# Performance work log

Measured on AMD Instinct MI355X. Metric: run time of the kernel, lower is better.

## Reference

```python
import jax, jax.numpy as jnp
import numpy as np

B, T, C, K = 8, 4096, 256, 4  # batch, time, d_embd, k_periods


def setup_inputs() -> dict:
    key = jax.random.key(0)
    ks = jax.random.split(key, 5)
    x = jax.random.normal(ks[0], (B, T, C), jnp.float32)
    # inception stand-in: masked 3x3 conv (HWIO) + GELU
    Wc = jax.random.normal(ks[1], (3, 3, C, C), jnp.float32) * 0.02
    bc = jnp.zeros((C,), jnp.float32)
    # FeedForward params
    W1 = jax.random.normal(ks[2], (C, 4 * C), jnp.float32) * 0.02
    b1 = jnp.zeros((4 * C,), jnp.float32)
    W2 = jax.random.normal(ks[3], (4 * C, C), jnp.float32) * 0.02
    b2 = jnp.zeros((C,), jnp.float32)
    return {"x": x, "Wc": Wc, "bc": bc, "W1": W1, "b1": b1, "W2": W2, "b2": b2}


def _topk_freq_idx(x):
    # eager (concrete) period detection; shapes downstream are data-dependent,
    # exactly like the torch original (which is also not compilable as one graph)
    xf = jnp.fft.rfft(x, axis=1)[:, 1:, :]            # drop DC -> [B, T//2, C]
    amps_full = jnp.mean(jnp.abs(xf), axis=-1)        # [B, T//2]
    _, idx = jax.lax.top_k(amps_full, K)              # [B, K] indices into sliced bins
    return np.asarray(jax.device_get(idx))


def _fold(x, n):
    # vectorized per-sample 1D->2D folding with period n[b]; returns masked grid
    pad = (T - T % n) % n
    m = (T + pad) // n
    M, N = int(m.max()), int(n.max())
    nj = jnp.asarray(n)[:, None, None]                # [B,1,1]
    i = jnp.arange(M)[None, :, None]
    j = jnp.arange(N)[None, None, :]
    t = i * nj + j                                    # [B,M,N] flat time index
    valid = (j < nj) & (t < T)
    tc = jnp.clip(t, 0, T - 1)
    grid = x[jnp.arange(B)[:, None, None], tc] * valid[..., None]  # [B,M,N,C]
    mask = valid[..., None].astype(x.dtype)
    return grid, mask


def _inception(grid, mask, Wc, bc):
    y = jax.lax.conv_general_dilated(
        grid, Wc, window_strides=(1, 1), padding='SAME',
        dimension_numbers=('NHWC', 'HWIO', 'NHWC'))
    return jax.nn.gelu(y + bc, approximate=False) * mask


def _unfold(y, n):
    ts = jnp.arange(T)[None, :]
    nj = jnp.asarray(n)[:, None]
    return y[jnp.arange(B)[:, None], ts // nj, ts % nj]  # [B,T,C]


def _forward(x, Wc, bc, W1, b1, W2, b2, idx_np):
    # differentiable amplitude recomputation with fixed (closed-over) indices
    xf = jnp.fft.rfft(x, axis=1)[:, 1:, :]
    amps_full = jnp.mean(jnp.abs(xf), axis=-1)                     # [B, T//2]
    amps_k = jnp.take_along_axis(amps_full, jnp.asarray(idx_np), axis=1)  # [B,K]
    # original computes p = T // topk_index; clamp to avoid div-by-zero on idx 0
    p = np.maximum(T // np.maximum(idx_np, 1), 1)                   # [B,K] np ints
    outs = []
    for k in range(K):
        grid, mask = _fold(x, p[:, k])
        y = _inception(grid, mask, Wc, bc)
        outs.append(_unfold(y, p[:, k]))
    tf = jnp.stack(outs, axis=1)                                   # [B,K,T,C]
    h = jax.nn.gelu(tf @ W1 + b1, approximate=False) @ W2 + b2     # FeedForward
    w = jax.nn.softmax(amps_k, axis=-1)[:, :, None, None]
    return x + (h * w).sum(axis=1)


def reference(x, Wc, bc, W1, b1, W2, b2):
    idx_np = _topk_freq_idx(x)
    return _forward(x, Wc, bc, W1, b1, W2, b2, idx_np)
```

## Files before the change

### kernel.cpp

```cpp
#include <hip/hip_runtime.h>
#include <cstdint>
#include <cstddef>

#define T_LEN 4096
#define C_DIM 256
#define B_DIM 8
#define K_TOP 4

typedef __attribute__((ext_vector_type(8))) short bf16x8;
typedef __attribute__((ext_vector_type(4))) float f32x4;

__device__ __forceinline__ float gelu_fast(float x) {
    float x2 = x * x;
    float a = x * fmaf(0.071354816f, x2, 1.595769122f);
    float e = __expf(-a);
    return __fdividef(x, 1.0f + e);
}

__device__ __forceinline__ unsigned short f2bf(float f) {
    uint32_t u = __float_as_uint(f);
    uint32_t r = (u + 0x7fffu + ((u >> 16) & 1u)) >> 16;
    return (unsigned short)r;
}

__device__ __forceinline__ float bf2f(unsigned short v) {
    uint32_t u = ((uint32_t)v) << 16;
    return __uint_as_float(u);
}

typedef __attribute__((address_space(3))) uint32_t lds_u32_t;
typedef __attribute__((address_space(1))) const uint32_t gbl_u32_t;

__device__ __forceinline__ void lds_load16(const void* g, void* l) {
    __builtin_amdgcn_global_load_lds((gbl_u32_t*)g, (lds_u32_t*)l, 16, 0, 0);
}

#define BAR_VM0()                                                      \
    do {                                                               \
        asm volatile("s_waitcnt vmcnt(0) lgkmcnt(0)" ::: "memory");    \
        __builtin_amdgcn_s_barrier();                                  \
        __builtin_amdgcn_sched_barrier(0);                             \
    } while (0)
#define BAR_VM3()                                                      \
    do {                                                               \
        asm volatile("s_waitcnt vmcnt(3) lgkmcnt(0)" ::: "memory");    \
        __builtin_amdgcn_s_barrier();                                  \
        __builtin_amdgcn_sched_barrier(0);                             \
    } while (0)
#define BAR_LGKM()                                                     \
    do {                                                               \
        asm volatile("s_waitcnt lgkmcnt(0)" ::: "memory");             \
        __builtin_amdgcn_s_barrier();                                  \
        __builtin_amdgcn_sched_barrier(0);                             \
    } while (0)

#define FPAD(i) ((i) + ((i) >> 5))

__global__ __launch_bounds__(256) void cvt_x_kernel(const float4* __restrict__ x,
                                                    ushort4* __restrict__ xbf,
                                                    unsigned short* __restrict__ zbuf) {
    size_t i = (size_t)blockIdx.x * 256 + threadIdx.x;
    float4 v = x[i];
    ushort4 o;
    o.x = f2bf(v.x); o.y = f2bf(v.y); o.z = f2bf(v.z); o.w = f2bf(v.w);
    xbf[i] = o;
    if (blockIdx.x == 0 && threadIdx.x < 256) zbuf[threadIdx.x] = 0;
}

__global__ __launch_bounds__(256) void transpose_cvtx_kernel(const float* __restrict__ x,
                                                             float* __restrict__ xT,
                                                             unsigned short* __restrict__ xbf,
                                                             unsigned short* __restrict__ zbuf) {
    __shared__ float tile[32][33];
    const int b = blockIdx.z;
    const int t0 = blockIdx.x * 32, c0 = blockIdx.y * 32;
    const int lx = threadIdx.x & 31, ly = threadIdx.x >> 5;
    const float* xp = x + (size_t)b * T_LEN * C_DIM;
    unsigned short* xbp = xbf + (size_t)b * T_LEN * C_DIM;
    float* op = xT + (size_t)b * C_DIM * T_LEN;
    for (int rr = ly; rr < 32; rr += 8) {
        float v = xp[(size_t)(t0 + rr) * C_DIM + c0 + lx];
        tile[rr][lx] = v;
        xbp[(size_t)(t0 + rr) * C_DIM + c0 + lx] = f2bf(v);
    }
    __syncthreads();
    for (int rr = ly; rr < 32; rr += 8)
        op[(size_t)(c0 + rr) * T_LEN + t0 + lx] = tile[lx][rr];
    if (blockIdx.x == 0 && blockIdx.y == 0 && blockIdx.z == 0)
        zbuf[threadIdx.x] = 0;
}

__global__ __launch_bounds__(256) void transpose_cvt_kernel(const float* __restrict__ src,
                                                            unsigned short* __restrict__ dst,
                                                            int R, int C) {
    __shared__ float t[32][33];
    const int c0 = blockIdx.x * 32, r0 = blockIdx.y * 32;
    const int lx = threadIdx.x & 31, ly = threadIdx.x >> 5;
    for (int rr = ly; rr < 32; rr += 8) {
        int r = r0 + rr, c = c0 + lx;
        t[rr][lx] = (r < R && c < C) ? src[(size_t)r * C + c] : 0.0f;
    }
    __syncthreads();
    for (int rr = ly; rr < 32; rr += 8) {
        int c = c0 + rr, r = r0 + lx;
        if (r < R && c < C) dst[(size_t)c * R + r] = f2bf(t[lx][rr]);
    }
}

__global__ __launch_bounds__(256) void repack_frag_kernel(const float* __restrict__ src,
                                                          unsigned short* __restrict__ dst,
                                                          int K, int N) {
    int idx = blockIdx.x * 256 + threadIdx.x;
    int total = (N >> 4) * (K >> 5) * 64;
    if (idx >= total) return;
    int lane = idx & 63, tile = idx >> 6;
    int ktiles = K >> 5;
    int tile_n = tile / ktiles, tile_k = tile % ktiles;
    int col = tile_n * 16 + (lane & 15);
    int k0 = tile_k * 32 + (lane >> 4) * 8;
    __align__(16) unsigned short v[8];
#pragma unroll
    for (int j = 0; j < 8; j++) v[j] = f2bf(src[(size_t)(k0 + j) * N + col]);
    *(uint4*)(dst + (size_t)idx * 8) = *(const uint4*)v;
}

__global__ __launch_bounds__(256) void fft_mag_kernel(const float* __restrict__ src,
                                                      unsigned short* __restrict__ mags,
                                                      int transposed) {
    const int bx = blockIdx.x;
    const int b = bx >> 8;
    const int c = bx & 255;
    const int tid = threadIdx.x;

    __shared__ __align__(16) float re[4224];
    __shared__ __align__(16) float im[4224];
    __shared__ __align__(16) float twr[2048];
    __shared__ __align__(16) float twi[2048];

    for (int u = tid; u < 2048; u += 256) {
        float ang = -6.283185307179586f * (float)u / 4096.0f;
        float s, co;
        sincosf(ang, &s, &co);
        twr[u] = co;
        twi[u] = s;
    }
    for (int i = tid; i < 4224; i += 256) im[i] = 0.0f;

    if (transposed) {
        const float4* row = (const float4*)(src + ((size_t)(b * C_DIM + c)) * T_LEN);
        for (int e4 = tid; e4 < 1024; e4 += 256) {
            float4 v = row[e4];
            int e = e4 * 4;
            re[FPAD((int)(__brev((unsigned)(e + 0)) >> 20))] = v.x;
            re[FPAD((int)(__brev((unsigned)(e + 1)) >> 20))] = v.y;
            re[FPAD((int)(__brev((unsigned)(e + 2)) >> 20))] = v.z;
            re[FPAD((int)(__brev((unsigned)(e + 3)) >> 20))] = v.w;
        }
    } else {
        const float* xp = src + (size_t)b * T_LEN * C_DIM + c;
        for (int e = tid; e < 4096; e += 256) {
            int r = (int)(__brev((unsigned)e) >> 20);
            re[FPAD(r)] = xp[(size_t)e * C_DIM];
        }
    }
    __syncthreads();

#pragma unroll
    for (int sp = 0; sp < 6; sp++) {
        const int h = 1 << (2 * sp);
        const int t1s = 11 - 2 * sp;
        const int t2s = 10 - 2 * sp;
        for (int j = tid; j < 1024; j += 256) {
            int p = j & (h - 1);
            int G = j >> (2 * sp);
            int base = G * 4 * h + p;
            int iA = FPAD(base), iB = FPAD(base + h);
            int iC = FPAD(base + 2 * h), iD = FPAD(base + 3 * h);
            float w1r = twr[p << t1s], w1i = twi[p << t1s];
            float w2r = twr[p << t2s], w2i = twi[p << t2s];
            float Ar = re[iA], Ai = im[iA], Br = re[iB], Bi = im[iB];
            float Cr = re[iC], Ci = im[iC], Dr = re[iD], Di = im[iD];
            float tBr = w1r * Br - w1i * Bi, tBi = w1r * Bi + w1i * Br;
            float tDr = w1r * Dr - w1i * Di, tDi = w1r * Di + w1i * Dr;
            float A1r = Ar + tBr, A1i = Ai + tBi;
            float B1r = Ar - tBr, B1i = Ai - tBi;
            float C1r = Cr + tDr, C1i = Ci + tDi;
            float D1r = Cr - tDr, D1i = Ci - tDi;
            float tCr = w2r * C1r - w2i * C1i, tCi = w2r * C1i + w2i * C1r;
            float uDr = w2r * D1r - w2i * D1i, uDi = w2r * D1i + w2i * D1r;
            float vDr = uDi, vDi = -uDr;
            re[iA] = A1r + tCr; im[iA] = A1i + tCi;
            re[iC] = A1r - tCr; im[iC] = A1i - tCi;
            re[iB] = B1r + vDr; im[iB] = B1i + vDi;
            re[iD] = B1r - vDr; im[iD] = B1i - vDi;
        }
        __syncthreads();
    }

    unsigned short* mp = mags + ((size_t)(b * C_DIM + c)) * 2048;
    for (int u = tid; u < 2048; u += 256) {
        int f = FPAD(u + 1);
        mp[u] = f2bf(sqrtf(re[f] * re[f] + im[f] * im[f]));
    }
}

__global__ __launch_bounds__(256) void reduce_amps_kernel(const unsigned short* __restrict__ mags,
                                                          float* __restrict__ partial) {
    const int b = blockIdx.z, cc = blockIdx.y;
    const int u = blockIdx.x * 256 + threadIdx.x;
    const unsigned short* mp = mags + ((size_t)b * C_DIM + cc * 32) * 2048 + u;
    float s = 0.0f;
    for (int c = 0; c < 32; c++) s += bf2f(mp[(size_t)c * 2048]);
    partial[((size_t)b * 8 + cc) * 2048 + u] = s;
}

__global__ __launch_bounds__(256) void topk_kernel(const float* __restrict__ partial,
                                                   int* __restrict__ meta_p,
                                                   float* __restrict__ meta_w) {
    const int b = blockIdx.x;
    const int tid = threadIdx.x;
    __shared__ float v[2048];
    __shared__ float rv[256];
    __shared__ int ri[256];
    __shared__ float topv[K_TOP];
    __shared__ int topi[K_TOP];

    for (int u = tid; u < 2048; u += 256) {
        float s = 0.0f;
        for (int cc = 0; cc < 8; cc++) s += partial[((size_t)b * 8 + cc) * 2048 + u];
        v[u] = s * (1.0f / (float)C_DIM);
    }

    for (int k = 0; k < K_TOP; k++) {
        __syncthreads();
        float bv = -1e30f;
        int bi = 2048;
        for (int u = tid; u < 2048; u += 256) {
            float val = v[u];
            if (val > bv) { bv = val; bi = u; }
        }
        rv[tid] = bv;
        ri[tid] = bi;
        __syncthreads();
        for (int s = 128; s > 0; s >>= 1) {
            if (tid < s) {
                float ov = rv[tid + s];
                int oi = ri[tid + s];
                if (ov > rv[tid] || (ov == rv[tid] && oi < ri[tid])) {
                    rv[tid] = ov;
                    ri[tid] = oi;
                }
            }
            __syncthreads();
        }
        if (tid == 0) {
            topv[k] = rv[0];
            topi[k] = ri[0];
            v[ri[0]] = -1e30f;
        }
    }
    __syncthreads();
    if (tid == 0) {
        float mx = topv[0];
        for (int k = 1; k < K_TOP; k++) mx = fmaxf(mx, topv[k]);
        float e[K_TOP], se = 0.0f;
        for (int k = 0; k < K_TOP; k++) { e[k] = expf(topv[k] - mx); se += e[k]; }
        for (int k = 0; k < K_TOP; k++) {
            int idx = topi[k];
            int d = (idx >= 1) ? idx : 1;
            int p = T_LEN / d;
            if (p < 1) p = 1;
            meta_p[b * K_TOP + k] = p;
            meta_w[b * K_TOP + k] = e[k] / se;
        }
    }
}

__global__ __launch_bounds__(512) void conv_mfma_kernel(const unsigned short* __restrict__ xbf,
                                                        const unsigned short* __restrict__ WcT,
                                                        const float* __restrict__ bc,
                                                        const int* __restrict__ meta_p,
                                                        const unsigned short* __restrict__ zbuf,
                                                        unsigned short* __restrict__ convbufs,
                                                        size_t conv_stride, int koff) {
    const int b = blockIdx.y;
    const int kz = blockIdx.z;
    const int n = meta_p[b * K_TOP + koff + kz];
    const int row0 = blockIdx.x * 128;
    const int tid = threadIdx.x, w = tid >> 6, lane = tid & 63;
    const int wm = w >> 2, wn = w & 3;

    __shared__ __align__(16) unsigned short Al[3][128 * 32];
    __shared__ __align__(16) unsigned short Bl[3][256 * 32];

    const int ra = tid >> 2;
    const int swz = ((tid & 3) ^ ((ra >> 1) & 3)) * 8;
    int ti, tj;
    {
        int t = row0 + ra;
        ti = t / n;
        tj = t - ti * n;
    }
    const unsigned short* xb = xbf + (size_t)b * T_LEN * C_DIM;
    const unsigned short* baseB0 = WcT + (size_t)ra * 2304 + swz;
    const unsigned short* baseB1 = WcT + (size_t)(ra + 128) * 2304 + swz;

    auto computeA = [&](int q) -> const unsigned short* {
        int di = q / 3 - 1, dj = q % 3 - 1;
        int ii = ti + di, jj = tj + dj;
        int tp = ii * n + jj;
        bool ok = (jj >= 0) && (jj < n) && (ii >= 0) && (tp < T_LEN);
        return ok ? (xb + (size_t)tp * C_DIM + swz) : (zbuf + swz);
    };

    f32x4 acc[4][4];
#pragma unroll
    for (int m = 0; m < 4; m++)
#pragma unroll
        for (int nn = 0; nn < 4; nn++) acc[m][nn] = (f32x4){0.f, 0.f, 0.f, 0.f};

    const unsigned short* baseA = computeA(0);
    lds_load16(baseA, &Al[0][tid * 8]);
    lds_load16(baseB0, &Bl[0][tid * 8]);
    lds_load16(baseB1, &Bl[0][4096 + tid * 8]);
    lds_load16(baseA + 32, &Al[1][tid * 8]);
    lds_load16(baseB0 + 32, &Bl[1][tid * 8]);
    lds_load16(baseB1 + 32, &Bl[1][4096 + tid * 8]);

    int cur = 0, stb = 2;
    for (int s = 0; s < 72; s++) {
        if (s < 71) BAR_VM3();
        else        BAR_VM0();

        const int t = s + 2;
        if (t < 72) {
            if ((t & 7) == 0) baseA = computeA(t >> 3);
            lds_load16(baseA + (t & 7) * 32, &Al[stb][tid * 8]);
            lds_load16(baseB0 + (size_t)t * 32, &Bl[stb][tid * 8]);
            lds_load16(baseB1 + (size_t)t * 32, &Bl[stb][4096 + tid * 8]);
        }

        bf16x8 af[4], bfr[4];
#pragma unroll
        for (int m = 0; m < 4; m++) {
            int row = wm * 64 + m * 16 + (lane & 15);
            af[m] = *(const bf16x8*)((const char*)&Al[cur][0] + row * 64 +
                                     (((lane >> 4) * 16) ^ (((row >> 1) & 3) << 4)));
        }
#pragma unroll
        for (int nn = 0; nn < 4; nn++) {
            int rowb = wn * 64 + nn * 16 + (lane & 15);
            bfr[nn] = *(const bf16x8*)((const char*)&Bl[cur][0] + rowb * 64 +
                                       (((lane >> 4) * 16) ^ (((rowb >> 1) & 3) << 4)));
        }
        __builtin_amdgcn_s_setprio(1);
#pragma unroll
        for (int m = 0; m < 4; m++)
#pragma unroll
            for (int nn = 0; nn < 4; nn++)
                acc[m][nn] = __builtin_amdgcn_mfma_f32_16x16x32_bf16(af[m], bfr[nn], acc[m][nn], 0, 0, 0);
        __builtin_amdgcn_s_setprio(0);

        cur = (cur == 2) ? 0 : cur + 1;
        stb = (stb == 2) ? 0 : stb + 1;
    }

    unsigned short* ob = convbufs + (size_t)kz * conv_stride + (size_t)b * T_LEN * C_DIM;
#pragma unroll
    for (int nn = 0; nn < 4; nn++) {
        int col = wn * 64 + nn * 16 + (lane & 15);
        float bs = bc[col];
#pragma unroll
        for (int m = 0; m < 4; m++) {
            int rbase = row0 + wm * 64 + m * 16 + (lane >> 4) * 4;
#pragma unroll
            for (int r = 0; r < 4; r++) {
                float v = acc[m][nn][r] + bs;
                ob[(size_t)(rbase + r) * C_DIM + col] = f2bf(gelu_fast(v));
            }
        }
    }
}

template <int KCNT>
__global__ __launch_bounds__(256, 2) void fused_ff_kernel(
    const unsigned short* __restrict__ convbufs, size_t conv_stride,
    const unsigned short* __restrict__ W1frag,
    const unsigned short* __restrict__ W2frag,
    const float* __restrict__ b1,
    const float* __restrict__ b2,
    const float* __restrict__ meta_w,
    float* __restrict__ out,
    const float* __restrict__ osrc,
    float b2scale, int koff) {
    const int tid = threadIdx.x;
    const int wn = tid >> 6, lane = tid & 63;
    const int row0 = blockIdx.x * 32;
    const int b = row0 >> 12;

    __shared__ __align__(16) unsigned short Asw[KCNT * 32 * 256];
    __shared__ __align__(16) unsigned short Hsw[2][32 * 128];

    float wkv[KCNT];
#pragma unroll
    for (int kc = 0; kc < KCNT; kc++) wkv[kc] = meta_w[b * K_TOP + koff + kc];

    {
        const unsigned short* base = convbufs + (size_t)row0 * C_DIM;
#pragma unroll
        for (int u = 0; u < KCNT * 4; u++) {
            int ch = u * 256 + tid;
            int rfull = ch >> 5;
            int kc = rfull >> 5;
            int trow = rfull & 31;
            int cole = ((ch & 31) * 8) ^ ((rfull & 7) << 3);
            lds_load16(base + (size_t)kc * conv_stride + (size_t)trow * 256 + cole,
                       (unsigned short*)Asw + (size_t)ch * 8);
        }
    }

    f32x4 acc2[2][4];
#pragma unroll
    for (int t2 = 0; t2 < 2; t2++)
#pragma unroll
        for (int nn = 0; nn < 4; nn++) acc2[t2][nn] = (f32x4){0.f, 0.f, 0.f, 0.f};

    BAR_VM0();

    for (int cc = 0; cc < 8; cc++) {
        const int par = cc & 1;

        f32x4 acc1[KCNT][2][2];
#pragma unroll
        for (int kc = 0; kc < KCNT; kc++)
#pragma unroll
            for (int n2 = 0; n2 < 2; n2++)
#pragma unroll
                for (int t2 = 0; t2 < 2; t2++) acc1[kc][n2][t2] = (f32x4){0.f, 0.f, 0.f, 0.f};

        __builtin_amdgcn_s_setprio(1);
#pragma unroll
        for (int ks = 0; ks < 8; ks++) {
            bf16x8 w1f[2];
#pragma unroll
            for (int n2 = 0; n2 < 2; n2++) {
                int tile_n = cc * 8 + wn * 2 + n2;
                w1f[n2] = *(const bf16x8*)(W1frag + ((size_t)(tile_n * 8 + ks) * 64 + lane) * 8);
            }
            bf16x8 af[KCNT][2];
#pragma unroll
            for (int kc = 0; kc < KCNT; kc++)
#pragma unroll
                for (int t2 = 0; t2 < 2; t2++) {
                    int row = kc * 32 + t2 * 16 + (lane & 15);
                    af[kc][t2] = *(const bf16x8*)((const char*)Asw + row * 512 +
                                                  ((ks * 64 + (lane >> 4) * 16) ^ ((row & 7) << 4)));
                }
#pragma unroll
            for (int kc = 0; kc < KCNT; kc++)
#pragma unroll
                for (int n2 = 0; n2 < 2; n2++)
#pragma unroll
                    for (int t2 = 0; t2 < 2; t2++)
                        acc1[kc][n2][t2] = __builtin_amdgcn_mfma_f32_16x16x32_bf16(
                            w1f[n2], af[kc][t2], acc1[kc][n2][t2], 0, 0, 0);
        }
        __builtin_amdgcn_s_setprio(0);

#pragma unroll
        for (int n2 = 0; n2 < 2; n2++) {
            const int hloc = wn * 32 + n2 * 16 + (lane >> 4) * 4;
            f32x4 bb = *(const f32x4*)(b1 + cc * 128 + hloc);
#pragma unroll
            for (int t2 = 0; t2 < 2; t2++) {
                float hc[4];
#pragma unroll
                for (int r = 0; r < 4; r++) {
                    float s = 0.0f;
#pragma unroll
                    for (int kc = 0; kc < KCNT; kc++)
                        s += wkv[kc] * gelu_fast(acc1[kc][n2][t2][r] + bb[r]);
                    hc[r] = s;
                }
                uint32_t lo, hi;
                asm("v_cvt_pk_bf16_f32 %0, %1, %2" : "=v"(lo) : "v"(hc[0]), "v"(hc[1]));
                asm("v_cvt_pk_bf16_f32 %0, %1, %2" : "=v"(hi) : "v"(hc[2]), "v"(hc[3]));
                uint2 pk;
                pk.x = lo;
                pk.y = hi;
                int t = t2 * 16 + (lane & 15);
                *(uint2*)((char*)&Hsw[par][0] + t * 256 +
                          ((hloc * 2) ^ ((t & 7) << 4))) = pk;
            }
        }
        BAR_LGKM();

        __builtin_amdgcn_s_setprio(1);
#pragma unroll
        for (int ks2 = 0; ks2 < 4; ks2++) {
            bf16x8 af2[2], w2f[4];
#pragma unroll
            for (int t2 = 0; t2 < 2; t2++) {
                int row = t2 * 16 + (lane & 15);
                af2[t2] = *(const bf16x8*)((const char*)&Hsw[par][0] + row * 256 +
                                           ((ks2 * 64 + (lane >> 4) * 16) ^ ((row & 7) << 4)));
            }
#pragma unroll
            for (int nn = 0; nn < 4; nn++) {
                int tile_n = wn * 4 + nn;
                int tile_k = cc * 4 + ks2;
                w2f[nn] = *(const bf16x8*)(W2frag + ((size_t)(tile_n * 32 + tile_k) * 64 + lane) * 8);
            }
#pragma unroll
            for (int t2 = 0; t2 < 2; t2++)
#pragma unroll
                for (int nn = 0; nn < 4; nn++)
                    acc2[t2][nn] = __builtin_amdgcn_mfma_f32_16x16x32_bf16(af2[t2], w2f[nn],
                                                                           acc2[t2][nn], 0, 0, 0);
        }
        __builtin_amdgcn_s_setprio(0);
    }

#pragma unroll
    for (int nn = 0; nn < 4; nn++) {
        int col = wn * 64 + nn * 16 + (lane & 15);
        float bb = b2scale * b2[col];
#pragma unroll
        for (int t2 = 0; t2 < 2; t2++) {
            int rbase = row0 + t2 * 16 + (lane >> 4) * 4;
#pragma unroll
            for (int r = 0; r < 4; r++) {
                size_t idx = (size_t)(rbase + r) * C_DIM + col;
                out[idx] = osrc[idx] + acc2[t2][nn][r] + bb;
            }
        }
    }
}

extern "C" void kernel_launch(void* const* d_in, const int* in_sizes, int n_in,
                              void* d_out, int out_size, void* d_ws, size_t ws_size,
                              hipStream_t stream) {
    const float* x  = (const float*)d_in[0];
    const float* Wc = (const float*)d_in[1];
    const float* bc = (const float*)d_in[2];
    const float* W1 = (const float*)d_in[3];
    const float* b1 = (const float*)d_in[4];
    const float* W2 = (const float*)d_in[5];
    const float* b2 = (const float*)d_in[6];
    float* out = (float*)d_out;

    const size_t CONV_ELEMS = (size_t)B_DIM * T_LEN * C_DIM;
    const size_t CONV_BYTES = CONV_ELEMS * 2;
    const size_t MAGS_BYTES = (size_t)B_DIM * C_DIM * 2048 * 2;
    const size_t XT_BYTES = (size_t)B_DIM * T_LEN * C_DIM * 4;

    uint8_t* ws = (uint8_t*)d_ws;
    size_t off = 0;
    auto alloc = [&](size_t bytes) {
        size_t o = off;
        off = (off + bytes + 255) & ~(size_t)255;
        return o;
    };
    float* partial = (float*)(ws + alloc((size_t)B_DIM * 8 * 2048 * 4));
    int* meta_p = (int*)(ws + alloc(B_DIM * K_TOP * 4));
    float* meta_w = (float*)(ws + alloc(B_DIM * K_TOP * 4));
    unsigned short* xbf = (unsigned short*)(ws + alloc((size_t)B_DIM * T_LEN * C_DIM * 2));
    unsigned short* WcT = (unsigned short*)(ws + alloc((size_t)256 * 2304 * 2));
    unsigned short* W1frag = (unsigned short*)(ws + alloc((size_t)256 * 1024 * 2));
    unsigned short* W2frag = (unsigned short*)(ws + alloc((size_t)1024 * 256 * 2));
    unsigned short* zbuf = (unsigned short*)(ws + alloc(512));

    size_t remaining = (ws_size > off) ? (ws_size - off) : 0;
    uint8_t* regionA = ws + off;
    int tier;
    if (remaining >= 4 * CONV_BYTES) tier = 2;
    else if (remaining >= MAGS_BYTES + XT_BYTES) tier = 1;
    else tier = 0;

    unsigned short* mags = (unsigned short*)regionA;
    float* xT = (float*)(regionA + ((tier == 2) ? CONV_BYTES : MAGS_BYTES));
    unsigned short* convbufs = (unsigned short*)regionA;
    const int use_xT = (tier >= 1);

    if (use_xT) {
        transpose_cvtx_kernel<<<dim3(T_LEN / 32, C_DIM / 32, B_DIM), 256, 0, stream>>>(
            x, xT, xbf, zbuf);
    } else {
        cvt_x_kernel<<<dim3((B_DIM * T_LEN * C_DIM / 4) / 256), 256, 0, stream>>>(
            (const float4*)x, (ushort4*)xbf, zbuf);
    }

    transpose_cvt_kernel<<<dim3(256 / 32, 2304 / 32), 256, 0, stream>>>(Wc, WcT, 2304, 256);
    repack_frag_kernel<<<dim3(128), 256, 0, stream>>>(W1, W1frag, 256, 1024);
    repack_frag_kernel<<<dim3(128), 256, 0, stream>>>(W2, W2frag, 1024, 256);

    if (use_xT) {
        fft_mag_kernel<<<dim3(B_DIM * C_DIM), 256, 0, stream>>>(xT, mags, 1);
    } else {
        fft_mag_kernel<<<dim3(B_DIM * C_DIM), 256, 0, stream>>>(x, mags, 0);
    }
    reduce_amps_kernel<<<dim3(2048 / 256, 8, B_DIM), 256, 0, stream>>>(mags, partial);
    topk_kernel<<<dim3(B_DIM), 256, 0, stream>>>(partial, meta_p, meta_w);

    if (tier == 2) {
        conv_mfma_kernel<<<dim3(32, B_DIM, K_TOP), 512, 0, stream>>>(
            xbf, WcT, bc, meta_p, zbuf, convbufs, CONV_ELEMS, 0);
        fused_ff_kernel<4><<<dim3(B_DIM * T_LEN / 32), 256, 0, stream>>>(
            convbufs, CONV_ELEMS, W1frag, W2frag, b1, b2, meta_w, out, x, 1.0f, 0);
    } else {
        for (int k = 0; k < K_TOP; k++) {
            conv_mfma_kernel<<<dim3(32, B_DIM, 1), 512, 0, stream>>>(
                xbf, WcT, bc, meta_p, zbuf, convbufs, 0, k);
            fused_ff_kernel<1><<<dim3(B_DIM * T_LEN / 32), 256, 0, stream>>>(
                convbufs, 0, W1frag, W2frag, b1, b2, meta_w, out,
                (k == 0) ? x : out, (k == K_TOP - 1) ? 1.0f : 0.0f, k);
        }
    }
}
```

Before: 385.1 us.

## Pack two real channels per complex FFT and store transposed x as bf16

The FFT magnitude pass now packs two real channels into one complex FFT, using the real and imaginary parts. Conjugate symmetry then separates the two spectra, which halves the number of FFT blocks. The transposed copy of x is also stored as bf16 instead of fp32, halving the bytes written by the transpose and read by the FFT. The cost is bf16 rounding of the FFT input, which could change which frequencies top-k selects when amplitudes are close.

Result: faster. 367.4 us (-4.6%).

```diff
diff --git a/kernel.cpp b/kernel.cpp
--- a/kernel.cpp
+++ b/kernel.cpp
@@ -68,7 +68,7 @@
 }
 
 __global__ __launch_bounds__(256) void transpose_cvtx_kernel(const float* __restrict__ x,
-                                                             float* __restrict__ xT,
+                                                             unsigned short* __restrict__ xTb,
                                                              unsigned short* __restrict__ xbf,
                                                              unsigned short* __restrict__ zbuf) {
     __shared__ float tile[32][33];
@@ -77,7 +77,7 @@
     const int lx = threadIdx.x & 31, ly = threadIdx.x >> 5;
     const float* xp = x + (size_t)b * T_LEN * C_DIM;
     unsigned short* xbp = xbf + (size_t)b * T_LEN * C_DIM;
-    float* op = xT + (size_t)b * C_DIM * T_LEN;
+    unsigned short* op = xTb + (size_t)b * C_DIM * T_LEN;
     for (int rr = ly; rr < 32; rr += 8) {
         float v = xp[(size_t)(t0 + rr) * C_DIM + c0 + lx];
         tile[rr][lx] = v;
@@ -85,26 +85,9 @@
     }
     __syncthreads();
     for (int rr = ly; rr < 32; rr += 8)
-        op[(size_t)(c0 + rr) * T_LEN + t0 + lx] = tile[lx][rr];
+        op[(size_t)(c0 + rr) * T_LEN + t0 + lx] = f2bf(tile[lx][rr]);
     if (blockIdx.x == 0 && blockIdx.y == 0 && blockIdx.z == 0)
         zbuf[threadIdx.x] = 0;
-}
-
-__global__ __launch_bounds__(256) void transpose_cvt_kernel(const float* __restrict__ src,
-                                                            unsigned short* __restrict__ dst,
-                                                            int R, int C) {
-    __shared__ float t[32][33];
-    const int c0 = blockIdx.x * 32, r0 = blockIdx.y * 32;
-    const int lx = threadIdx.x & 31, ly = threadIdx.x >> 5;
-    for (int rr = ly; rr < 32; rr += 8) {
-        int r = r0 + rr, c = c0 + lx;
-        t[rr][lx] = (r < R && c < C) ? src[(size_t)r * C + c] : 0.0f;
-    }
-    __syncthreads();
-    for (int rr = ly; rr < 32; rr += 8) {
-        int c = c0 + rr, r = r0 + lx;
-        if (r < R && c < C) dst[(size_t)c * R + r] = f2bf(t[lx][rr]);
-    }
 }
 
 __global__ __launch_bounds__(256) void repack_frag_kernel(const float* __restrict__ src,
@@ -124,12 +107,28 @@
     *(uint4*)(dst + (size_t)idx * 8) = *(const uint4*)v;
 }
 
-__global__ __launch_bounds__(256) void fft_mag_kernel(const float* __restrict__ src,
-                                                      unsigned short* __restrict__ mags,
-                                                      int transposed) {
+__global__ __launch_bounds__(256) void transpose_cvt_kernel(const float* __restrict__ src,
+                                                            unsigned short* __restrict__ dst,
+                                                            int R, int C) {
+    __shared__ float t[32][33];
+    const int c0 = blockIdx.x * 32, r0 = blockIdx.y * 32;
+    const int lx = threadIdx.x & 31, ly = threadIdx.x >> 5;
+    for (int rr = ly; rr < 32; rr += 8) {
+        int r = r0 + rr, c = c0 + lx;
+        t[rr][lx] = (r < R && c < C) ? src[(size_t)r * C + c] : 0.0f;
+    }
+    __syncthreads();
+    for (int rr = ly; rr < 32; rr += 8) {
+        int c = c0 + rr, r = r0 + lx;
+        if (r < R && c < C) dst[(size_t)c * R + r] = f2bf(t[lx][rr]);
+    }
+}
+
+__global__ __launch_bounds__(256) void fft_mag_pair_kernel(const unsigned short* __restrict__ xTb,
+                                                           unsigned short* __restrict__ mags) {
     const int bx = blockIdx.x;
-    const int b = bx >> 8;
-    const int c = bx & 255;
+    const int b = bx >> 7;
+    const int c0 = (bx & 127) * 2;
     const int tid = threadIdx.x;
 
     __shared__ __align__(16) float re[4224];
@@ -144,23 +143,21 @@
         twr[u] = co;
         twi[u] = s;
     }
-    for (int i = tid; i < 4224; i += 256) im[i] = 0.0f;
-
-    if (transposed) {
-        const float4* row = (const float4*)(src + ((size_t)(b * C_DIM + c)) * T_LEN);
-        for (int e4 = tid; e4 < 1024; e4 += 256) {
-            float4 v = row[e4];
-            int e = e4 * 4;
-            re[FPAD((int)(__brev((unsigned)(e + 0)) >> 20))] = v.x;
-            re[FPAD((int)(__brev((unsigned)(e + 1)) >> 20))] = v.y;
-            re[FPAD((int)(__brev((unsigned)(e + 2)) >> 20))] = v.z;
-            re[FPAD((int)(__brev((unsigned)(e + 3)) >> 20))] = v.w;
-        }
-    } else {
-        const float* xp = src + (size_t)b * T_LEN * C_DIM + c;
-        for (int e = tid; e < 4096; e += 256) {
-            int r = (int)(__brev((unsigned)e) >> 20);
-            re[FPAD(r)] = xp[(size_t)e * C_DIM];
+
+    {
+        const uint4* r0 = (const uint4*)(xTb + ((size_t)(b * C_DIM + c0)) * T_LEN);
+        const uint4* r1 = (const uint4*)(xTb + ((size_t)(b * C_DIM + c0 + 1)) * T_LEN);
+        for (int e8 = tid; e8 < 512; e8 += 256) {
+            uint4 v0 = r0[e8], v1 = r1[e8];
+            const unsigned short* p0 = (const unsigned short*)&v0;
+            const unsigned short* p1 = (const unsigned short*)&v1;
+            int e = e8 * 8;
+#pragma unroll
+            for (int j = 0; j < 8; j++) {
+                int r = (int)(__brev((unsigned)(e + j)) >> 20);
+                re[FPAD(r)] = bf2f(p0[j]);
+                im[FPAD(r)] = bf2f(p1[j]);
+            }
         }
     }
     __syncthreads();
@@ -197,6 +194,81 @@
         __syncthreads();
     }
 
+    unsigned short* mp0 = mags + ((size_t)(b * C_DIM + c0)) * 2048;
+    unsigned short* mp1 = mp0 + 2048;
+    for (int u = tid; u < 2048; u += 256) {
+        int f = u + 1;
+        int g = 4096 - f;
+        int jf = FPAD(f), jg = FPAD(g);
+        float ar = re[jf], ai = im[jf];
+        float br = re[jg], bi = im[jg];
+        float xr = ar + br, xi = ai - bi;
+        float yr = ai + bi, yi = br - ar;
+        mp0[u] = f2bf(0.5f * sqrtf(xr * xr + xi * xi));
+        mp1[u] = f2bf(0.5f * sqrtf(yr * yr + yi * yi));
+    }
+}
+
+__global__ __launch_bounds__(256) void fft_mag_kernel(const float* __restrict__ src,
+                                                      unsigned short* __restrict__ mags) {
+    const int bx = blockIdx.x;
+    const int b = bx >> 8;
+    const int c = bx & 255;
+    const int tid = threadIdx.x;
+
+    __shared__ __align__(16) float re[4224];
+    __shared__ __align__(16) float im[4224];
+    __shared__ __align__(16) float twr[2048];
+    __shared__ __align__(16) float twi[2048];
+
+    for (int u = tid; u < 2048; u += 256) {
+        float ang = -6.283185307179586f * (float)u / 4096.0f;
+        float s, co;
+        sincosf(ang, &s, &co);
+        twr[u] = co;
+        twi[u] = s;
+    }
+    for (int i = tid; i < 4224; i += 256) im[i] = 0.0f;
+
+    const float* xp = src + (size_t)b * T_LEN * C_DIM + c;
+    for (int e = tid; e < 4096; e += 256) {
+        int r = (int)(__brev((unsigned)e) >> 20);
+        re[FPAD(r)] = xp[(size_t)e * C_DIM];
+    }
+    __syncthreads();
+
+#pragma unroll
+    for (int sp = 0; sp < 6; sp++) {
+        const int h = 1 << (2 * sp);
+        const int t1s = 11 - 2 * sp;
+        const int t2s = 10 - 2 * sp;
+        for (int j = tid; j < 1024; j += 256) {
+            int p = j & (h - 1);
+            int G = j >> (2 * sp);
+            int base = G * 4 * h + p;
+            int iA = FPAD(base), iB = FPAD(base + h);
+            int iC = FPAD(base + 2 * h), iD = FPAD(base + 3 * h);
+            float w1r = twr[p << t1s], w1i = twi[p << t1s];
+            float w2r = twr[p << t2s], w2i = twi[p << t2s];
+            float Ar = re[iA], Ai = im[iA], Br = re[iB], Bi = im[iB];
+            float Cr = re[iC], Ci = im[iC], Dr = re[iD], Di = im[iD];
+            float tBr = w1r * Br - w1i * Bi, tBi = w1r * Bi + w1i * Br;
+            float tDr = w1r * Dr - w1i * Di, tDi = w1r * Di + w1i * Dr;
+            float A1r = Ar + tBr, A1i = Ai + tBi;
+            float B1r = Ar - tBr, B1i = Ai - tBi;
+            float C1r = Cr + tDr, C1i = Ci + tDi;
+            float D1r = Cr - tDr, D1i = Ci - tDi;
+            float tCr = w2r * C1r - w2i * C1i, tCi = w2r * C1i + w2i * C1r;
+            float uDr = w2r * D1r - w2i * D1i, uDi = w2r * D1i + w2i * D1r;
+            float vDr = uDi, vDi = -uDr;
+            re[iA] = A1r + tCr; im[iA] = A1i + tCi;
+            re[iC] = A1r - tCr; im[iC] = A1i - tCi;
+            re[iB] = B1r + vDr; im[iB] = B1i + vDi;
+            re[iD] = B1r - vDr; im[iD] = B1i - vDi;
+        }
+        __syncthreads();
+    }
+
     unsigned short* mp = mags + ((size_t)(b * C_DIM + c)) * 2048;
     for (int u = tid; u < 2048; u += 256) {
         int f = FPAD(u + 1);
@@ -552,7 +624,7 @@
     const size_t CONV_ELEMS = (size_t)B_DIM * T_LEN * C_DIM;
     const size_t CONV_BYTES = CONV_ELEMS * 2;
     const size_t MAGS_BYTES = (size_t)B_DIM * C_DIM * 2048 * 2;
-    const size_t XT_BYTES = (size_t)B_DIM * T_LEN * C_DIM * 4;
+    const size_t XT_BYTES = (size_t)B_DIM * T_LEN * C_DIM * 2;
 
     uint8_t* ws = (uint8_t*)d_ws;
     size_t off = 0;
@@ -578,13 +650,13 @@
     else tier = 0;
 
     unsigned short* mags = (unsigned short*)regionA;
-    float* xT = (float*)(regionA + ((tier == 2) ? CONV_BYTES : MAGS_BYTES));
+    unsigned short* xTb = (unsigned short*)(regionA + ((tier == 2) ? CONV_BYTES : MAGS_BYTES));
     unsigned short* convbufs = (unsigned short*)regionA;
     const int use_xT = (tier >= 1);
 
     if (use_xT) {
         transpose_cvtx_kernel<<<dim3(T_LEN / 32, C_DIM / 32, B_DIM), 256, 0, stream>>>(
-            x, xT, xbf, zbuf);
+            x, xTb, xbf, zbuf);
     } else {
         cvt_x_kernel<<<dim3((B_DIM * T_LEN * C_DIM / 4) / 256), 256, 0, stream>>>(
             (const float4*)x, (ushort4*)xbf, zbuf);
@@ -595,9 +667,9 @@
     repack_frag_kernel<<<dim3(128), 256, 0, stream>>>(W2, W2frag, 1024, 256);
 
     if (use_xT) {
-        fft_mag_kernel<<<dim3(B_DIM * C_DIM), 256, 0, stream>>>(xT, mags, 1);
+        fft_mag_pair_kernel<<<dim3(B_DIM * 128), 256, 0, stream>>>(xTb, mags);
     } else {
-        fft_mag_kernel<<<dim3(B_DIM * C_DIM), 256, 0, stream>>>(x, mags, 0);
+        fft_mag_kernel<<<dim3(B_DIM * C_DIM), 256, 0, stream>>>(x, mags);
     }
     reduce_amps_kernel<<<dim3(2048 / 256, 8, B_DIM), 256, 0, stream>>>(mags, partial);
     topk_kernel<<<dim3(B_DIM), 256, 0, stream>>>(partial, meta_p, meta_w);
```
